# Optimization experiments

Measured on AMD Instinct MI355X. Metric: run time of the kernel, lower is better.

The kernel has to match this reference:

```python
import jax, jax.numpy as jnp
import numpy as np

B_SZ, C, H, W = 64, 256, 28, 28
HEADS, HEAD_DIM = 4, 64
BLOCK, HALO = 4, 4
WIN = BLOCK + 2 * HALO  # 12
KCONV = 3


def _unfold(x, k, s, p):
    # torch F.unfold semantics; returns [b, c, oh, kh, ow, kw]
    b, c, h, w = x.shape
    xp = jnp.pad(x, ((0, 0), (0, 0), (p, p), (p, p)))
    oh = (h + 2 * p - k) // s + 1
    ow = (w + 2 * p - k) // s + 1
    ih = jnp.arange(oh)[:, None] * s + jnp.arange(k)[None, :]
    iw = jnp.arange(ow)[:, None] * s + jnp.arange(k)[None, :]
    pt = xp[:, :, ih]            # [b,c,oh,kh,Wp]
    pt = pt[:, :, :, :, iw]      # [b,c,oh,kh,ow,kw]
    return pt


def _rel_to_abs(x):
    # x: [b, l, 2r-1] -> [b, l, r] via shift trick
    b, l, m = x.shape
    r = (m + 1) // 2
    x = jnp.pad(x, ((0, 0), (0, 0), (0, 1))).reshape(b, l * (m + 1))
    x = jnp.pad(x, ((0, 0), (0, m - l))).reshape(b, l + 1, m)
    return x[:, :l, -r:]


def _relative_logits_1d(q, rel_k):
    # q: [b, x, y, d], rel_k: [2r-1, d] -> [b, x, i(=r), y, j(=r)]
    b, h, w, _ = q.shape
    r = (rel_k.shape[0] + 1) // 2
    logits = jnp.einsum('bxyd,rd->bxyr', q, rel_k)
    logits = _rel_to_abs(logits.reshape(b * h, w, 2 * r - 1)).reshape(b, h, w, r)
    return jnp.broadcast_to(logits[:, :, None], (b, h, r, w, r))


def _rel_pos_emb(q, rel_height, rel_width):
    # q: [B, block^2, d]
    B, n, d = q.shape
    qb = q.reshape(B, BLOCK, BLOCK, d)
    lw = _relative_logits_1d(qb, rel_width)                 # [B,x,i,y,j]
    lw = lw.transpose(0, 1, 3, 2, 4).reshape(B, n, -1)      # b (x y) (i j)
    qh = qb.transpose(0, 2, 1, 3)
    lh = _relative_logits_1d(qh, rel_height)                # [B,y,i,x,j]
    lh = lh.transpose(0, 3, 1, 4, 2).reshape(B, n, -1)      # b (y x) (j i)
    return lw + lh


def setup_inputs() -> dict:
    key = jax.random.key(0)
    ks = jax.random.split(key, 13)
    f = jnp.float32
    rel_scale = HEAD_DIM ** (-0.5)
    return {
        'x': jax.random.normal(ks[0], (B_SZ, C, H, W), dtype=f),
        'w1': jax.random.normal(ks[1], (C, C), dtype=f) * 0.05,
        'b1': jax.random.normal(ks[2], (C,), dtype=f) * 0.05,
        'w2': jax.random.normal(ks[3], (C, C), dtype=f) * 0.05,
        'b2': jax.random.normal(ks[4], (C,), dtype=f) * 0.05,
        'w3': jax.random.normal(ks[5], (C, C), dtype=f) * 0.05,
        'b3': jax.random.normal(ks[6], (C,), dtype=f) * 0.05,
        'fc_w': jax.random.normal(ks[7], (KCONV * KCONV, 3 * HEADS), dtype=f) * 0.1,
        'dep_w': jax.random.normal(ks[8], (C, KCONV * KCONV, KCONV, KCONV), dtype=f) * 0.05,
        'rel_height': jax.random.normal(ks[9], (2 * WIN - 1, HEAD_DIM), dtype=f) * rel_scale,
        'rel_width': jax.random.normal(ks[10], (2 * WIN - 1, HEAD_DIM), dtype=f) * rel_scale,
        'rate1': jax.random.normal(ks[11], (1,), dtype=f),
        'rate2': jax.random.normal(ks[12], (1,), dtype=f),
    }


def reference(x, w1, b1, w2, b2, w3, b3, fc_w, dep_w, rel_height, rel_width, rate1, rate2):
    b = x.shape[0]
    scaling = HEAD_DIM ** (-0.5)
    q = jnp.einsum('bchw,oc->bohw', x, w1) + b1[None, :, None, None]
    k = jnp.einsum('bchw,oc->bohw', x, w2) + b2[None, :, None, None]
    v = jnp.einsum('bchw,oc->bohw', x, w3) + b3[None, :, None, None]
    c = q.shape[1]
    nb = H // BLOCK          # 7 blocks per side
    nwin = nb * nb           # 49 windows
    n_q = BLOCK * BLOCK      # 16 queries per window
    n_k = WIN * WIN          # 144 keys per window (with halo)

    # block queries: b c (h p1) (w p2) -> (b h w) (p1 p2) c
    q_att = q.reshape(b, c, nb, BLOCK, nb, BLOCK).transpose(0, 2, 4, 3, 5, 1).reshape(b * nwin, n_q, c)
    kp = _unfold(k, WIN, BLOCK, HALO).transpose(0, 2, 4, 3, 5, 1).reshape(b * nwin, n_k, c)
    vp = _unfold(v, WIN, BLOCK, HALO).transpose(0, 2, 4, 3, 5, 1).reshape(b * nwin, n_k, c)

    def split_heads(t):
        Bn, n, _ = t.shape
        return t.reshape(Bn, n, HEADS, HEAD_DIM).transpose(0, 2, 1, 3).reshape(Bn * HEADS, n, HEAD_DIM)

    q1 = split_heads(q_att) * scaling
    k1 = split_heads(kp)
    v1 = split_heads(vp)

    sim = jnp.einsum('bid,bjd->bij', q1, k1)
    sim = sim + _rel_pos_emb(q1, rel_height, rel_width)

    # NOTE: faithfully reproduces original (valid positions get -max, padded get 0)
    ones = jnp.ones((1, 1, H, W), x.dtype)
    valid = _unfold(ones, WIN, BLOCK, HALO).transpose(0, 2, 4, 3, 5, 1).reshape(nwin, n_k) > 0
    big_neg = -jnp.finfo(sim.dtype).max
    sim = sim.reshape(b, nwin, HEADS, n_q, n_k)
    sim = jnp.where(valid[None, :, None, None, :], big_neg, sim)
    attn = jax.nn.softmax(sim, axis=-1).reshape(b * nwin * HEADS, n_q, n_k)

    out = jnp.einsum('bij,bjd->bid', attn, v1)
    out = out.reshape(b * nwin, HEADS, n_q, HEAD_DIM).transpose(0, 2, 1, 3)  # merge heads
    out = out.reshape(b, nb, nb, BLOCK, BLOCK, c)
    out_att = out.transpose(0, 5, 1, 3, 2, 4).reshape(b, c, H, W)

    # conv branch: fc over concatenated per-head q,k,v, then depthwise-grouped conv
    f_all = jnp.concatenate([
        q.reshape(b, HEADS, HEAD_DIM, H * W),
        k.reshape(b, HEADS, HEAD_DIM, H * W),
        v.reshape(b, HEADS, HEAD_DIM, H * W)], axis=1)        # [b, 3*heads, hd, HW]
    f_all = jnp.einsum('bcmn,oc->bomn', f_all, fc_w)          # [b, 9, hd, HW]
    f_conv = f_all.transpose(0, 2, 1, 3).reshape(b, HEAD_DIM * KCONV * KCONV, H, W)
    out_conv = jax.lax.conv_general_dilated(
        f_conv, dep_w, window_strides=(1, 1), padding=((1, 1), (1, 1)),
        dimension_numbers=('NCHW', 'OIHW', 'NCHW'), feature_group_count=HEAD_DIM)

    return rate1[0] * out_att + rate2[0] * out_conv
```

## Files before the change

kernel.cpp:

```cpp
#include <hip/hip_runtime.h>
#include <hip/hip_bf16.h>

typedef __hip_bfloat16 bf16;
typedef unsigned int uint;
typedef unsigned short ushort;

using frag8 = __attribute__((ext_vector_type(8))) short;
using f32x4 = __attribute__((ext_vector_type(4))) float;

#define HWH 784
#define PPITCH 30
#define PPLANE 900
#define PBLK 10800

__global__ __launch_bounds__(256) void fold_w2(const float* __restrict__ fc_w,
                                               const float* __restrict__ dep_w,
                                               const float* __restrict__ b1,
                                               const float* __restrict__ b2,
                                               const float* __restrict__ b3,
                                               float* __restrict__ W2,
                                               float* __restrict__ biascat) {
    int idx = blockIdx.x * 256 + threadIdx.x;
    if (idx < 768) {
        const float* bs = idx < 256 ? b1 : (idx < 512 ? b2 : b3);
        biascat[idx] = bs[idx & 255];
    }
    if (idx >= 256 * 108) return;
    int oc  = idx / 108;
    int r   = idx % 108;
    int c12 = r / 9;
    int k9  = r % 9;
    float s = 0.f;
#pragma unroll
    for (int o = 0; o < 9; ++o)
        s += fc_w[o * 12 + c12] * dep_w[oc * 81 + o * 9 + k9];
    W2[idx] = s;
}

__global__ __launch_bounds__(256) void wprep(const float* __restrict__ w1,
                                             const float* __restrict__ w2,
                                             const float* __restrict__ w3,
                                             bf16* __restrict__ wbf) {
    int row = blockIdx.x, tid = threadIdx.x;
    const float* src = row < 256 ? w1 : (row < 512 ? w2 : w3);
    wbf[row * 256 + tid] = __float2bfloat16(src[(row & 255) * 256 + tid]);
}

__global__ __launch_bounds__(256) void xpose(const float* __restrict__ x,
                                             bf16* __restrict__ xT) {
    __shared__ float t[32][33];
    const int n0 = blockIdx.x * 32, c0 = blockIdx.y * 32, b = blockIdx.z;
    const int tid = threadIdx.x;
    const float* xb = x + (size_t)b * (256 * HWH);
#pragma unroll
    for (int e = tid; e < 1024; e += 256) {
        int r = e >> 5, col = e & 31;
        int n = n0 + col;
        t[r][col] = (n < HWH) ? xb[(size_t)(c0 + r) * HWH + n] : 0.f;
    }
    __syncthreads();
#pragma unroll
    for (int e = tid; e < 512; e += 256) {
        int r = e >> 4, cp = (e & 15) * 2;
        int n = n0 + r;
        if (n < HWH) {
            __hip_bfloat162 h;
            h.x = __float2bfloat16(t[cp][r]);
            h.y = __float2bfloat16(t[cp + 1][r]);
            *reinterpret_cast<__hip_bfloat162*>(
                &xT[((size_t)b * HWH + n) * 256 + c0 + cp]) = h;
        }
    }
}

__device__ inline void load_lds16(const bf16* g, short* lds) {
    __builtin_amdgcn_global_load_lds(
        (const __attribute__((address_space(1))) void*)g,
        (__attribute__((address_space(3))) void*)lds, 16, 0, 0);
}

__global__ __launch_bounds__(256) void gemm_mfma(const bf16* __restrict__ wbf,
                                                 const float* __restrict__ biascat,
                                                 const bf16* __restrict__ xT,
                                                 bf16* __restrict__ perm) {
    __shared__ short ldsB[16384];

    const int tid  = threadIdx.x;
    const int wave = tid >> 6, lane = tid & 63;
    const int b    = blockIdx.y;
    const int n0   = blockIdx.x * 64;
    const int lrow = lane & 15, lkc = lane >> 4;

    const bf16* xb = xT + (size_t)b * (HWH * 256);

#pragma unroll
    for (int si = 0; si < 8; ++si) {
        const int s = wave * 8 + si;
        const int kc = s >> 2, jb = s & 3;
        int n = n0 + jb * 16 + lrow;
        if (n > HWH - 1) n = HWH - 1;
        const bf16* gb = xb + (size_t)n * 256 + kc * 32 + lkc * 8;
        load_lds16(gb, &ldsB[s * 512]);
    }
    __syncthreads();

#pragma unroll 1
    for (int mt = 0; mt < 6; ++mt) {
        f32x4 acc[2][4] = {};
        const int rowbase = mt * 128 + wave * 32 + lrow;
#pragma unroll 2
        for (int kc = 0; kc < 8; ++kc) {
            frag8 a[2], bb[4];
#pragma unroll
            for (int i = 0; i < 2; ++i)
                a[i] = *reinterpret_cast<const frag8*>(
                    &wbf[(size_t)(rowbase + i * 16) * 256 + kc * 32 + lkc * 8]);
#pragma unroll
            for (int j = 0; j < 4; ++j)
                bb[j] = *reinterpret_cast<const frag8*>(
                    &ldsB[(kc * 4 + j) * 512 + lane * 8]);
#pragma unroll
            for (int i = 0; i < 2; ++i)
#pragma unroll
                for (int j = 0; j < 4; ++j)
                    acc[i][j] = __builtin_amdgcn_mfma_f32_16x16x32_bf16(
                        a[i], bb[j], acc[i][j], 0, 0, 0);
        }

#pragma unroll
        for (int i = 0; i < 2; ++i) {
            const int rowb = mt * 128 + wave * 32 + i * 16 + lkc * 4;
            bf16* base[4]; float bias4[4];
#pragma unroll
            for (int r = 0; r < 4; ++r) {
                const int m = rowb + r;
                const int sec = m >> 8, ch = m & 255;
                base[r] = perm + ((size_t)b * 64 + (ch & 63)) * PBLK
                               + (size_t)(sec * 4 + (ch >> 6)) * PPLANE;
                bias4[r] = biascat[m];
            }
#pragma unroll
            for (int j = 0; j < 4; ++j) {
                const int col = n0 + j * 16 + lrow;
                if (col < HWH) {
                    const int pos = col + 2 * (col / 28) + 31;
#pragma unroll
                    for (int r = 0; r < 4; ++r)
                        base[r][pos] = __float2bfloat16(acc[i][j][r] + bias4[r]);
                }
            }
        }
    }
}

__global__ __launch_bounds__(256) void attmean(const bf16* __restrict__ perm,
                                               const float* __restrict__ rate1,
                                               float* __restrict__ attm) {
    const int b = blockIdx.y, cg = blockIdx.x;
    const int wave = threadIdx.x >> 6, lane = threadIdx.x & 63;
    const int c = cg * 4 + wave;
    const bf16* vp = perm + ((size_t)(b * 64 + (c & 63)) * 12 + 8 + (c >> 6)) * (size_t)PPLANE;

    float cs[5] = {0.f, 0.f, 0.f, 0.f, 0.f};
    if (lane < 28) {
#pragma unroll
        for (int y = 0; y < 28; ++y) {
            float v = __bfloat162float(vp[(y + 1) * PPITCH + lane + 1]);
#pragma unroll
            for (int wi = 0; wi < 5; ++wi)
                if (y >= 4 * wi && y <= 4 * wi + 11) cs[wi] += v;
        }
    }
    const float r1s = rate1[0] * (1.0f / 144.0f);
#pragma unroll
    for (int wi = 0; wi < 5; ++wi) {
        float p = cs[wi];
#pragma unroll
        for (int d = 1; d < 32; d <<= 1) {
            float t = __shfl_up(p, d);
            if (lane >= d) p += t;
        }
        float hi = __shfl(p, 4 * lane + 11);
        float lo = __shfl(p, 4 * lane - 1);
        if (lane < 5) {
            float w = hi - (lane ? lo : 0.f);
            attm[((size_t)b * 256 + c) * 25 + wi * 5 + lane] = w * r1s;
        }
    }
}

__global__ __launch_bounds__(256) void out_fused5(
    const bf16* __restrict__ perm, const float* __restrict__ W2,
    const float* __restrict__ attm, const float* __restrict__ rate2,
    float* __restrict__ out) {
    __shared__ __align__(16) short planes[12 * PPLANE];
    __shared__ float w2s[4][12][12];
    __shared__ float attbs[4][25];

    const int g = blockIdx.x, b = blockIdx.y, tid = threadIdx.x;

    const uint4* src = (const uint4*)(perm + (size_t)(b * 64 + g) * PBLK);
#pragma unroll
    for (int it = 0; it < 6; ++it) {
        int e = tid + it * 256;
        if (e < 1350) ((uint4*)planes)[e] = src[e];
    }
    for (int e = tid; e < 576; e += 256) {
        int oc = e / 144, rem = e % 144, cc = rem / 12, k = rem % 12;
        w2s[oc][cc][k] = (k < 9) ? W2[(4 * g + oc) * 108 + cc * 9 + k] : 0.f;
    }
    if (tid < 100)
        attbs[tid / 25][tid % 25] =
            attm[((size_t)b * 256 + 4 * g + tid / 25) * 25 + tid % 25];
    __syncthreads();

    for (int e = tid; e < 1392; e += 256) {
        int c12 = e / 116, u = e % 116, idx;
        if (u < 30)      idx = u;
        else if (u < 60) idx = 870 + (u - 30);
        else { int v = u - 60; idx = ((v >> 1) + 1) * PPITCH + (v & 1) * 29; }
        planes[c12 * PPLANE + idx] = 0;
    }
    __syncthreads();

    float acc[4][4] = {};
    const int y = tid % 28, xs = tid / 28, x0 = xs * 4;
    if (tid < 196) {
#pragma unroll 1
        for (int c = 0; c < 12; ++c) {
            float rr[3][6];
#pragma unroll
            for (int dy = 0; dy < 3; ++dy) {
                const uint* row = (const uint*)&planes[c * PPLANE + (y + dy) * PPITCH + x0];
#pragma unroll
                for (int jp = 0; jp < 3; ++jp) {
                    uint w = row[jp];
                    float2 f = __bfloat1622float2(*(const __hip_bfloat162*)&w);
                    rr[dy][2 * jp]     = f.x;
                    rr[dy][2 * jp + 1] = f.y;
                }
            }
#pragma unroll
            for (int oc = 0; oc < 4; ++oc) {
                const float4* wr = reinterpret_cast<const float4*>(&w2s[oc][c][0]);
                float4 wa = wr[0], wb = wr[1], wc = wr[2];
                const float wk[9] = {wa.x, wa.y, wa.z, wa.w, wb.x, wb.y, wb.z, wb.w, wc.x};
#pragma unroll
                for (int ky = 0; ky < 3; ++ky)
#pragma unroll
                    for (int kx = 0; kx < 3; ++kx) {
                        float wv = wk[ky * 3 + kx];
#pragma unroll
                        for (int px = 0; px < 4; ++px)
                            acc[oc][px] += wv * rr[ky][px + kx];
                    }
            }
        }

        const float r2 = rate2[0];
        const int wi = (y >> 2) - 1, wj = xs - 1;
        const bool inter = (wi >= 0) & (wi < 5) & (wj >= 0) & (wj < 5);
#pragma unroll
        for (int oc = 0; oc < 4; ++oc) {
            float av = inter ? attbs[oc][wi * 5 + wj] : 0.f;
            float4 o;
            o.x = av + r2 * acc[oc][0];
            o.y = av + r2 * acc[oc][1];
            o.z = av + r2 * acc[oc][2];
            o.w = av + r2 * acc[oc][3];
            *reinterpret_cast<float4*>(
                &out[((size_t)(b * 256 + 4 * g + oc)) * HWH + y * 28 + x0]) = o;
        }
    }
}

extern "C" void kernel_launch(void* const* d_in, const int* in_sizes, int n_in,
                              void* d_out, int out_size, void* d_ws, size_t ws_size,
                              hipStream_t stream) {
    const float* x     = (const float*)d_in[0];
    const float* w1    = (const float*)d_in[1];
    const float* b1    = (const float*)d_in[2];
    const float* w2    = (const float*)d_in[3];
    const float* b2    = (const float*)d_in[4];
    const float* w3    = (const float*)d_in[5];
    const float* b3    = (const float*)d_in[6];
    const float* fc_w  = (const float*)d_in[7];
    const float* dep_w = (const float*)d_in[8];
    const float* rate1 = (const float*)d_in[11];
    const float* rate2 = (const float*)d_in[12];
    float* out = (float*)d_out;

    char* wsb = (char*)d_ws;
    bf16*  perm    = (bf16*)wsb;
    bf16*  xT      = (bf16*)(wsb + 88473600);
    float* attm    = (float*)(wsb + 88473600);
    bf16*  wbf     = (bf16*)(wsb + 114163712);
    float* W2      = (float*)(wsb + 114556928);
    float* biascat = (float*)(wsb + 114667520);

    fold_w2   <<<dim3(108),        dim3(256), 0, stream>>>(fc_w, dep_w, b1, b2, b3, W2, biascat);
    wprep     <<<dim3(768),        dim3(256), 0, stream>>>(w1, w2, w3, wbf);
    xpose     <<<dim3(25, 8, 64),  dim3(256), 0, stream>>>(x, xT);
    gemm_mfma <<<dim3(13, 64),     dim3(256), 0, stream>>>(wbf, biascat, xT, perm);
    attmean   <<<dim3(64, 64),     dim3(256), 0, stream>>>(perm, rate1, attm);
    out_fused5<<<dim3(64, 64),     dim3(256), 0, stream>>>(perm, W2, attm, rate2, out);
}
```

Before: 274.5 us.

## Split GEMM M-tiles across grid and prefetch A fragments in the MFMA loop

The gemm_mfma kernel now launches three times as many blocks, each handling two of the six 128-row M tiles instead of all six. This raises parallelism from 832 to 2496 blocks. The cost is that each block reloads its B tile (xT slice) into LDS, tripling that traffic. The A-fragment global loads are also software-prefetched one k-step ahead to hide latency behind the MFMAs.

```diff
diff --git a/kernel.cpp b/kernel.cpp
--- a/kernel.cpp
+++ b/kernel.cpp
@@ -87,7 +87,8 @@
 
     const int tid  = threadIdx.x;
     const int wave = tid >> 6, lane = tid & 63;
-    const int b    = blockIdx.y;
+    const int b    = blockIdx.z;
+    const int mc   = blockIdx.y;
     const int n0   = blockIdx.x * 64;
     const int lrow = lane & 15, lkc = lane >> 4;
 
@@ -105,26 +106,33 @@
     __syncthreads();
 
 #pragma unroll 1
-    for (int mt = 0; mt < 6; ++mt) {
+    for (int mti = 0; mti < 2; ++mti) {
+        const int mt = mc * 2 + mti;
         f32x4 acc[2][4] = {};
         const int rowbase = mt * 128 + wave * 32 + lrow;
+        const bf16* aptr = wbf + (size_t)rowbase * 256 + lkc * 8;
+
+        frag8 a0 = *reinterpret_cast<const frag8*>(&aptr[0]);
+        frag8 a1 = *reinterpret_cast<const frag8*>(&aptr[16 * 256]);
 #pragma unroll 2
         for (int kc = 0; kc < 8; ++kc) {
-            frag8 a[2], bb[4];
-#pragma unroll
-            for (int i = 0; i < 2; ++i)
-                a[i] = *reinterpret_cast<const frag8*>(
-                    &wbf[(size_t)(rowbase + i * 16) * 256 + kc * 32 + lkc * 8]);
+            const frag8 ac0 = a0, ac1 = a1;
+            if (kc < 7) {
+                a0 = *reinterpret_cast<const frag8*>(&aptr[(kc + 1) * 32]);
+                a1 = *reinterpret_cast<const frag8*>(&aptr[16 * 256 + (kc + 1) * 32]);
+            }
+            frag8 bb[4];
 #pragma unroll
             for (int j = 0; j < 4; ++j)
                 bb[j] = *reinterpret_cast<const frag8*>(
                     &ldsB[(kc * 4 + j) * 512 + lane * 8]);
 #pragma unroll
-            for (int i = 0; i < 2; ++i)
-#pragma unroll
-                for (int j = 0; j < 4; ++j)
-                    acc[i][j] = __builtin_amdgcn_mfma_f32_16x16x32_bf16(
-                        a[i], bb[j], acc[i][j], 0, 0, 0);
+            for (int j = 0; j < 4; ++j) {
+                acc[0][j] = __builtin_amdgcn_mfma_f32_16x16x32_bf16(
+                    ac0, bb[j], acc[0][j], 0, 0, 0);
+                acc[1][j] = __builtin_amdgcn_mfma_f32_16x16x32_bf16(
+                    ac1, bb[j], acc[1][j], 0, 0, 0);
+            }
         }
 
 #pragma unroll
@@ -301,7 +309,7 @@
     fold_w2   <<<dim3(108),        dim3(256), 0, stream>>>(fc_w, dep_w, b1, b2, b3, W2, biascat);
     wprep     <<<dim3(768),        dim3(256), 0, stream>>>(w1, w2, w3, wbf);
     xpose     <<<dim3(25, 8, 64),  dim3(256), 0, stream>>>(x, xT);
-    gemm_mfma <<<dim3(13, 64),     dim3(256), 0, stream>>>(wbf, biascat, xT, perm);
+    gemm_mfma <<<dim3(13, 3, 64),  dim3(256), 0, stream>>>(wbf, biascat, xT, perm);
     attmean   <<<dim3(64, 64),     dim3(256), 0, stream>>>(perm, rate1, attm);
     out_fused5<<<dim3(64, 64),     dim3(256), 0, stream>>>(perm, W2, attm, rate2, out);
 }
```

After: 264.5 us. 3.6% less time.
